# Performance work log

Hardware: AMD Instinct MI355X
Metric: run time of the kernel (lower is better)

Reference implementation:

```python
import math
import jax, jax.numpy as jnp
import numpy as np

B, T, C = 4, 2048, 1024
N_HEAD = 16
HEAD_DIM = C // N_HEAD

def setup_inputs() -> dict:
    key = jax.random.key(0)
    k0, k1, k2, k3, k4 = jax.random.split(key, 5)
    s = 1.0 / math.sqrt(C)
    return {
        "x": jax.random.normal(k0, (B, T, C), dtype=jnp.float32),
        "W_q": jax.random.normal(k1, (C, C), dtype=jnp.float32) * s,
        "W_k": jax.random.normal(k2, (C, C), dtype=jnp.float32) * s,
        "W_v": jax.random.normal(k3, (C, C), dtype=jnp.float32) * s,
        "W_o": jax.random.normal(k4, (C, C), dtype=jnp.float32) * s,
    }

def reference(x, W_q, W_k, W_v, W_o):
    b, t, c = x.shape
    h, hd = N_HEAD, HEAD_DIM
    # nn.Linear(y) = y @ W.T ; project and split heads -> [B, H, T, hd]
    q = (x @ W_q.T).reshape(b, t, h, hd).transpose(0, 2, 1, 3)
    k = (x @ W_k.T).reshape(b, t, h, hd).transpose(0, 2, 1, 3)
    v = (x @ W_v.T).reshape(b, t, h, hd).transpose(0, 2, 1, 3)
    # scores [B, H, T, T], causal mask, stable softmax
    attn = jnp.einsum('bhqd,bhkd->bhqk', q, k) / math.sqrt(hd)
    causal = jnp.tril(jnp.ones((t, t), dtype=bool))
    attn = jnp.where(causal[None, None], attn, -jnp.inf)
    attn = jax.nn.softmax(attn, axis=-1)
    out = jnp.einsum('bhqk,bhkd->bhqd', attn, v)
    out = out.transpose(0, 2, 1, 3).reshape(b, t, c)
    return out @ W_o.T
```

## Files before the change

kernel.cpp:

```cpp
#include <hip/hip_runtime.h>
#include <math.h>

#define Bsz 4
#define Tsz 2048
#define Csz 1024
#define NH  16
#define HD  64

typedef short bf16x8 __attribute__((ext_vector_type(8)));
typedef float f32x4  __attribute__((ext_vector_type(4)));
typedef unsigned short u16;
typedef unsigned int uint;

__device__ __forceinline__ u16 f2bf(float f) {
    union { float f; unsigned u; } v; v.f = f;
    unsigned r = v.u + 0x7fffu + ((v.u >> 16) & 1u);
    return (u16)(r >> 16);
}

__device__ __forceinline__ uint pkbf(float a, float b) {
    union { float f; uint u; } x, y; x.f = a; y.f = b;
    return ((x.u + 0x8000u) >> 16) | ((y.u + 0x8000u) & 0xFFFF0000u);
}

__device__ __forceinline__ void glds16(const u16* g, u16* l) {
    __builtin_amdgcn_global_load_lds(
        (const __attribute__((address_space(1))) void*)g,
        (__attribute__((address_space(3))) void*)l, 16, 0, 0);
}

__global__ void cast_kernel(const float* __restrict__ src, u16* __restrict__ dst, int n) {
    int i = (blockIdx.x * blockDim.x + threadIdx.x) * 8;
    if (i + 8 <= n) {
        float4 a = *(const float4*)(src + i);
        float4 b = *(const float4*)(src + i + 4);
        bf16x8 o;
        o[0] = (short)f2bf(a.x); o[1] = (short)f2bf(a.y);
        o[2] = (short)f2bf(a.z); o[3] = (short)f2bf(a.w);
        o[4] = (short)f2bf(b.x); o[5] = (short)f2bf(b.y);
        o[6] = (short)f2bf(b.z); o[7] = (short)f2bf(b.w);
        *(bf16x8*)(dst + i) = o;
    } else {
        for (; i < n; i++) dst[i] = f2bf(src[i]);
    }
}

__global__ void cast4_kernel(const float* __restrict__ s0, const float* __restrict__ s1,
                             const float* __restrict__ s2, const float* __restrict__ s3,
                             u16* __restrict__ dst) {
    const int NW = Csz * Csz;
    int i = (blockIdx.x * blockDim.x + threadIdx.x) * 8;
    int m = i >> 20;
    int local = i & (NW - 1);
    const float* src = (m == 0) ? s0 : (m == 1) ? s1 : (m == 2) ? s2 : s3;
    float4 a = *(const float4*)(src + local);
    float4 b = *(const float4*)(src + local + 4);
    bf16x8 o;
    o[0] = (short)f2bf(a.x); o[1] = (short)f2bf(a.y);
    o[2] = (short)f2bf(a.z); o[3] = (short)f2bf(a.w);
    o[4] = (short)f2bf(b.x); o[5] = (short)f2bf(b.y);
    o[6] = (short)f2bf(b.z); o[7] = (short)f2bf(b.w);
    *(bf16x8*)(dst + i) = o;
}


#define G2_SS 24576

#define G2_STAGEA(SLOT, KH, KT, PTR) {                                               \
    const int row_ = tid >> 2;                                                       \
    const int sc_ = (tid & 3) ^ ((row_ >> 1) & 3);                                   \
    glds16((PTR) + (size_t)row_ * 1024 + (KT) * 64 + (KH) * 32 + sc_ * 8,            \
           lds + (SLOT) * G2_SS + (KH) * 4096 + wave * 512); }

#define G2_STAGEB(SLOT, KH, KT, PTR) {                                               \
    _Pragma("unroll")                                                                \
    for (int rho = 0; rho < 2; rho++) {                                              \
        const int row_ = rho * 128 + (tid >> 2);                                     \
        const int sc_ = (tid & 3) ^ ((row_ >> 1) & 3);                               \
        glds16((PTR) + (size_t)row_ * 1024 + (KT) * 64 + (KH) * 32 + sc_ * 8,        \
               lds + (SLOT) * G2_SS + 8192 + (KH) * 8192 + rho * 4096 + wave * 512); } }

#define G2_PHASE(SLOT, KH, STAGE)                                                    \
    {                                                                                \
        __builtin_amdgcn_s_barrier();                                                \
        asm volatile("" ::: "memory");                                               \
        STAGE                                                                        \
        const u16* abase = lds + (SLOT) * G2_SS + (KH) * 4096;                       \
        const u16* bbase = lds + (SLOT) * G2_SS + 8192 + (KH) * 8192;                \
        bf16x8 afr[4], bfr[4];                                                       \
        _Pragma("unroll")                                                            \
        for (int i = 0; i < 4; i++) {                                                \
            const int ar = wrb + i * 16 + lr;                                        \
            afr[i] = *(const bf16x8*)(abase + ar * 32 +                              \
                                      ((lq ^ ((ar >> 1) & 3)) * 8));                 \
        }                                                                            \
        _Pragma("unroll")                                                            \
        for (int j = 0; j < 4; j++) {                                                \
            const int nr = wcb + j * 16 + lr;                                        \
            bfr[j] = *(const bf16x8*)(bbase + nr * 32 +                              \
                                      ((lq ^ ((nr >> 1) & 3)) * 8));                 \
        }                                                                            \
        asm volatile("" ::: "memory");                                               \
        __builtin_amdgcn_s_setprio(1);                                               \
        _Pragma("unroll")                                                            \
        for (int i = 0; i < 4; i++)                                                  \
            _Pragma("unroll")                                                        \
            for (int j = 0; j < 4; j++)                                              \
                acc[i][j] = __builtin_amdgcn_mfma_f32_16x16x32_bf16(                 \
                    afr[i], bfr[j], acc[i][j], 0, 0, 0);                             \
        __builtin_amdgcn_s_setprio(0);                                               \
    }

#define G2_VM(N) asm volatile("s_waitcnt vmcnt(" #N ")" ::: "memory")

#define G2_BODY(AP_, BP_)                                                            \
    __shared__ u16 lds[49152];                                                       \
    const int tid = threadIdx.x;                                                     \
    const int wave = tid >> 6, lane = tid & 63;                                      \
    const int lr = lane & 15, lq = lane >> 4;                                        \
    const int wrb = (wave >> 2) * 64, wcb = (wave & 3) * 64;                         \
    f32x4 acc[4][4] = {};                                                            \
    G2_STAGEA(0, 0, 0, AP_) G2_STAGEB(0, 0, 0, BP_)                                  \
    G2_STAGEA(0, 1, 0, AP_) G2_STAGEB(0, 1, 0, BP_)                                  \
    G2_STAGEA(1, 0, 1, AP_) G2_STAGEB(1, 0, 1, BP_)                                  \
    for (int t = 0; t < 16; t++) {                                                   \
        const int s = t & 1;                                                         \
        if (t == 15) { G2_VM(3); } else { G2_VM(6); }                                \
        G2_PHASE(s, 0, if (t < 15) { G2_STAGEA(s ^ 1, 1, t + 1, AP_)                 \
                                     G2_STAGEB(s ^ 1, 1, t + 1, BP_) })              \
        if (t == 15) { G2_VM(0); } else { G2_VM(6); }                                \
        G2_PHASE(s, 1, if (t < 14) { G2_STAGEA(s, 0, t + 2, AP_)                     \
                                     G2_STAGEB(s, 0, t + 2, BP_) })                  \
    }

__global__ __launch_bounds__(512, 2)
void gemm_qkv(const u16* __restrict__ A, const u16* __restrict__ Bm,
              u16* __restrict__ Qo, u16* __restrict__ Ko, u16* __restrict__ Vo,
              float qscale) {
    const int wg = blockIdx.x;
    const int chunk = wg & 7, pos = wg >> 3;
    const int m0 = ((chunk >> 1) * 16 + pos / 6) * 128;
    const int n0 = ((chunk & 1) * 6 + pos % 6) * 256;
    const u16* Ap = A  + (size_t)m0 * 1024;
    const u16* Bp = Bm + (size_t)n0 * 1024;

    G2_BODY(Ap, Bp)

    const int sel = n0 >> 10;
    if (sel == 2) {
        #pragma unroll
        for (int mi = 0; mi < 4; mi++) {
            #pragma unroll
            for (int ni = 0; ni < 4; ni++) {
                int m = m0 + wrb + mi * 16 + lq * 4;
                int b = m >> 11, tt = m & (Tsz - 1);
                int n = (n0 & 1023) + wcb + ni * 16 + lr;
                int h = n >> 6, d = n & (HD - 1);
                uint2 pk;
                pk.x = pkbf(acc[mi][ni][0], acc[mi][ni][1]);
                pk.y = pkbf(acc[mi][ni][2], acc[mi][ni][3]);
                *(uint2*)(&Vo[(((size_t)b * NH + h) * HD + d) * Tsz + tt]) = pk;
            }
        }
    } else {
        const float scale = (sel == 0) ? qscale : 1.0f;
        u16* dst = (sel == 0) ? Qo : Ko;
        #pragma unroll
        for (int mi = 0; mi < 4; mi++)
            #pragma unroll
            for (int ni = 0; ni < 4; ni++)
                #pragma unroll
                for (int r = 0; r < 4; r++) {
                    int m = m0 + wrb + mi * 16 + lq * 4 + r;
                    int n = (n0 & 1023) + wcb + ni * 16 + lr;
                    int b = m >> 11, tt = m & (Tsz - 1);
                    int h = n >> 6,  d = n & (HD - 1);
                    dst[(((size_t)b * NH + h) * Tsz + tt) * HD + d] = f2bf(acc[mi][ni][r] * scale);
                }
    }
}

__global__ __launch_bounds__(512, 2)
void gemm_out(const u16* __restrict__ A, const u16* __restrict__ Bm,
              float* __restrict__ out) {
    const int wg = blockIdx.x;
    const int chunk = wg & 7, pos = wg >> 3;
    const int m0 = (chunk * 8 + (pos >> 2)) * 128;
    const int n0 = (pos & 3) * 256;
    const u16* Ap = A  + (size_t)m0 * 1024;
    const u16* Bp = Bm + (size_t)n0 * 1024;

    G2_BODY(Ap, Bp)

    #pragma unroll
    for (int mi = 0; mi < 4; mi++)
        #pragma unroll
        for (int ni = 0; ni < 4; ni++)
            #pragma unroll
            for (int r = 0; r < 4; r++) {
                int m = m0 + wrb + mi * 16 + lq * 4 + r;
                int n = n0 + wcb + ni * 16 + lr;
                out[(size_t)m * Csz + n] = acc[mi][ni][r];
            }
}

#define LDT  72
#define LDTP 68

__global__ __launch_bounds__(256, 4)
void attn_kernel(const u16* __restrict__ Q, const u16* __restrict__ Kb,
                 const u16* __restrict__ Vt, u16* __restrict__ O) {
    __shared__ u16 sK[64 * LDT];
    __shared__ u16 sV[64 * LDT];
    __shared__ u16 sP[4][16 * LDTP];
    const int tid  = threadIdx.x;
    const int wave = tid >> 6, lane = tid & 63;
    const int lr = lane & 15, lq = lane >> 4;
    const int bh = blockIdx.x;
    const int qa = blockIdx.y;
    const int qc = 31 - qa;
    const int ta = qa * 64, tc = qc * 64;

    const u16* Qp = Q  + (size_t)bh * Tsz * HD;
    const u16* Kp = Kb + (size_t)bh * Tsz * HD;
    const u16* Vp = Vt + (size_t)bh * HD * Tsz;

    bf16x8 qfA0 = *(const bf16x8*)(Qp + (size_t)(ta + wave * 16 + lr) * HD + lq * 8);
    bf16x8 qfA1 = *(const bf16x8*)(Qp + (size_t)(ta + wave * 16 + lr) * HD + 32 + lq * 8);
    bf16x8 qfC0 = *(const bf16x8*)(Qp + (size_t)(tc + wave * 16 + lr) * HD + lq * 8);
    bf16x8 qfC1 = *(const bf16x8*)(Qp + (size_t)(tc + wave * 16 + lr) * HD + 32 + lq * 8);

    f32x4 accOA[4] = {}, accOC[4] = {};
    f32x4 accLA = {}, accLC = {};

    bf16x8 ones;
    #pragma unroll
    for (int i = 0; i < 8; i++) ones[i] = (short)0x3F80;

    const int strow = tid >> 3;
    const int stcol = (tid & 7) * 8;
    const u16* gK0 = Kp + (size_t)strow * HD + stcol;
    const u16* gK1 = gK0 + 32 * HD;
    const u16* gV0 = Vp + (size_t)strow * Tsz + stcol;
    const u16* gV1 = gV0 + 32 * Tsz;
    u16* lK0 = sK + strow * LDT + stcol;  u16* lK1 = lK0 + 32 * LDT;
    u16* lV0 = sV + strow * LDT + stcol;  u16* lV1 = lV0 + 32 * LDT;

    bf16x8 pK0 = *(const bf16x8*)(gK0);
    bf16x8 pK1 = *(const bf16x8*)(gK1);
    bf16x8 pV0 = *(const bf16x8*)(gV0);
    bf16x8 pV1 = *(const bf16x8*)(gV1);

#define PROCESS(T0, QF0, QF1, ACCO, ACCL, DIAG)                                       \
    {                                                                                 \
        f32x4 accS[4];                                                                \
        __builtin_amdgcn_s_setprio(1);                                                \
        _Pragma("unroll")                                                             \
        for (int j = 0; j < 4; j++) {                                                 \
            bf16x8 b0 = *(const bf16x8*)(sK + (j * 16 + lr) * LDT + lq * 8);          \
            bf16x8 b1 = *(const bf16x8*)(sK + (j * 16 + lr) * LDT + 32 + lq * 8);     \
            f32x4 z = {};                                                             \
            z = __builtin_amdgcn_mfma_f32_16x16x32_bf16(QF0, b0, z, 0, 0, 0);         \
            z = __builtin_amdgcn_mfma_f32_16x16x32_bf16(QF1, b1, z, 0, 0, 0);         \
            accS[j] = z;                                                              \
        }                                                                             \
        __builtin_amdgcn_s_setprio(0);                                                \
        _Pragma("unroll")                                                             \
        for (int r = 0; r < 4; r++) {                                                 \
            const int rowg = (T0) + wave * 16 + lq * 4 + r;                           \
            _Pragma("unroll")                                                         \
            for (int j = 0; j < 4; j++) {                                             \
                float v = accS[j][r];                                                 \
                if (DIAG && (kb * 64 + j * 16 + lr > rowg)) v = -200.0f;              \
                union { float f; uint u; } e;                                         \
                e.f = __builtin_amdgcn_exp2f(v);                                      \
                sP[wave][(lq * 4 + r) * LDTP + j * 16 + lr] = (u16)(e.u >> 16);       \
            }                                                                         \
        }                                                                             \
        __builtin_amdgcn_s_setprio(1);                                                \
        _Pragma("unroll")                                                             \
        for (int ks = 0; ks < 2; ks++) {                                              \
            bf16x8 pf = *(const bf16x8*)(&sP[wave][0] + lr * LDTP + ks * 32 + lq * 8);\
            ACCL = __builtin_amdgcn_mfma_f32_16x16x32_bf16(pf, ones, ACCL, 0, 0, 0);  \
            _Pragma("unroll")                                                         \
            for (int j = 0; j < 4; j++) {                                             \
                bf16x8 vf = *(const bf16x8*)(sV + (j * 16 + lr) * LDT + ks * 32 + lq * 8); \
                ACCO[j] = __builtin_amdgcn_mfma_f32_16x16x32_bf16(pf, vf, ACCO[j], 0, 0, 0); \
            }                                                                         \
        }                                                                             \
        __builtin_amdgcn_s_setprio(0);                                                \
    }

    for (int kb = 0; kb <= qc; kb++) {
        __syncthreads();
        *(bf16x8*)lK0 = pK0; *(bf16x8*)lK1 = pK1;
        *(bf16x8*)lV0 = pV0; *(bf16x8*)lV1 = pV1;
        __syncthreads();
        if (kb < qc) {
            pK0 = *(const bf16x8*)(gK0 + (size_t)(kb + 1) * 64 * HD);
            pK1 = *(const bf16x8*)(gK1 + (size_t)(kb + 1) * 64 * HD);
            pV0 = *(const bf16x8*)(gV0 + (kb + 1) * 64);
            pV1 = *(const bf16x8*)(gV1 + (kb + 1) * 64);
        }
        if (kb < qa) {
            PROCESS(ta, qfA0, qfA1, accOA, accLA, 0)
            PROCESS(tc, qfC0, qfC1, accOC, accLC, 0)
        } else if (kb == qa) {
            PROCESS(ta, qfA0, qfA1, accOA, accLA, 1)
            PROCESS(tc, qfC0, qfC1, accOC, accLC, 0)
        } else if (kb < qc) {
            PROCESS(tc, qfC0, qfC1, accOC, accLC, 0)
        } else {
            PROCESS(tc, qfC0, qfC1, accOC, accLC, 1)
        }
    }
#undef PROCESS

    const int b = bh >> 4, h = bh & 15;
    #pragma unroll
    for (int j = 0; j < 4; j++) {
        #pragma unroll
        for (int r = 0; r < 4; r++) {
            int t = wave * 16 + lq * 4 + r;
            int d = j * 16 + lr;
            O[((size_t)b * Tsz + ta + t) * Csz + h * HD + d] = f2bf(accOA[j][r] / accLA[r]);
            O[((size_t)b * Tsz + tc + t) * Csz + h * HD + d] = f2bf(accOC[j][r] / accLC[r]);
        }
    }
}

extern "C" void kernel_launch(void* const* d_in, const int* in_sizes, int n_in,
                              void* d_out, int out_size, void* d_ws, size_t ws_size,
                              hipStream_t stream) {
    const float* x  = (const float*)d_in[0];
    const float* Wq = (const float*)d_in[1];
    const float* Wk = (const float*)d_in[2];
    const float* Wv = (const float*)d_in[3];
    const float* Wo = (const float*)d_in[4];
    float* out = (float*)d_out;

    const size_t NX = (size_t)Bsz * Tsz * Csz;
    const size_t NW = (size_t)Csz * Csz;

    char* ws = (char*)d_ws;
    u16* xb   = (u16*)ws; ws += NX * 2;
    u16* wqkv = (u16*)ws; ws += 3 * NW * 2;
    u16* wob  = (u16*)ws; ws += NW * 2;
    u16* qbuf = (u16*)ws; ws += NX * 2;
    u16* kbuf = (u16*)ws; ws += NX * 2;
    u16* vtb  = (u16*)ws; ws += NX * 2;
    u16* abuf = (u16*)ws; ws += NX * 2;

    cast_kernel<<<dim3((unsigned)(NX / 2048)), 256, 0, stream>>>(x, xb, (int)NX);
    cast4_kernel<<<dim3((unsigned)(4 * NW / 2048)), 256, 0, stream>>>(Wq, Wk, Wv, Wo, wqkv);

    const float qscale = 0.125f * 1.44269504088896340736f;
    gemm_qkv<<<dim3(768), 512, 0, stream>>>(xb, wqkv, qbuf, kbuf, vtb, qscale);

    attn_kernel<<<dim3(Bsz * NH, 16), 256, 0, stream>>>(qbuf, kbuf, vtb, abuf);

    gemm_out<<<dim3(256), 512, 0, stream>>>(abuf, wob, out);
}
```

Before: 258.1 us.

## Merge cast kernels, drop setprio hints, collapse attention branch dispatch

Fuses the activation and weight bf16 cast kernels into a single launch that picks its source by global index, removing one kernel launch. It also removes the s_setprio priority hints around the MFMA phases in the attention inner loop. The four-way branch over diagonal/non-diagonal tiles is replaced by two PROCESS calls with a runtime diagonal flag, which shrinks code size but makes the mask check a runtime condition instead of a compile-time constant.

```diff
diff --git a/kernel.cpp b/kernel.cpp
--- a/kernel.cpp
+++ b/kernel.cpp
@@ -29,38 +29,32 @@
         (__attribute__((address_space(3))) void*)l, 16, 0, 0);
 }
 
-__global__ void cast_kernel(const float* __restrict__ src, u16* __restrict__ dst, int n) {
-    int i = (blockIdx.x * blockDim.x + threadIdx.x) * 8;
-    if (i + 8 <= n) {
-        float4 a = *(const float4*)(src + i);
-        float4 b = *(const float4*)(src + i + 4);
-        bf16x8 o;
-        o[0] = (short)f2bf(a.x); o[1] = (short)f2bf(a.y);
-        o[2] = (short)f2bf(a.z); o[3] = (short)f2bf(a.w);
-        o[4] = (short)f2bf(b.x); o[5] = (short)f2bf(b.y);
-        o[6] = (short)f2bf(b.z); o[7] = (short)f2bf(b.w);
-        *(bf16x8*)(dst + i) = o;
+__global__ void cast_all(const float* __restrict__ x,
+                         const float* __restrict__ s0, const float* __restrict__ s1,
+                         const float* __restrict__ s2, const float* __restrict__ s3,
+                         u16* __restrict__ xb, u16* __restrict__ wdst) {
+    const int NW = Csz * Csz;
+    const size_t NX = (size_t)Bsz * Tsz * Csz;
+    size_t i = ((size_t)blockIdx.x * blockDim.x + threadIdx.x) * 8;
+    const float* src;
+    u16* dst;
+    if (i < NX) {
+        src = x + i; dst = xb + i;
     } else {
-        for (; i < n; i++) dst[i] = f2bf(src[i]);
-    }
-}
-
-__global__ void cast4_kernel(const float* __restrict__ s0, const float* __restrict__ s1,
-                             const float* __restrict__ s2, const float* __restrict__ s3,
-                             u16* __restrict__ dst) {
-    const int NW = Csz * Csz;
-    int i = (blockIdx.x * blockDim.x + threadIdx.x) * 8;
-    int m = i >> 20;
-    int local = i & (NW - 1);
-    const float* src = (m == 0) ? s0 : (m == 1) ? s1 : (m == 2) ? s2 : s3;
-    float4 a = *(const float4*)(src + local);
-    float4 b = *(const float4*)(src + local + 4);
+        size_t j = i - NX;
+        int m = (int)(j >> 20);
+        size_t local = j & (NW - 1);
+        src = ((m == 0) ? s0 : (m == 1) ? s1 : (m == 2) ? s2 : s3) + local;
+        dst = wdst + j;
+    }
+    float4 a = *(const float4*)(src);
+    float4 b = *(const float4*)(src + 4);
     bf16x8 o;
     o[0] = (short)f2bf(a.x); o[1] = (short)f2bf(a.y);
     o[2] = (short)f2bf(a.z); o[3] = (short)f2bf(a.w);
     o[4] = (short)f2bf(b.x); o[5] = (short)f2bf(b.y);
     o[6] = (short)f2bf(b.z); o[7] = (short)f2bf(b.w);
-    *(bf16x8*)(dst + i) = o;
+    *(bf16x8*)(dst) = o;
 }
 
 
@@ -254,7 +248,6 @@
 #define PROCESS(T0, QF0, QF1, ACCO, ACCL, DIAG)                                       \
     {                                                                                 \
         f32x4 accS[4];                                                                \
-        __builtin_amdgcn_s_setprio(1);                                                \
         _Pragma("unroll")                                                             \
         for (int j = 0; j < 4; j++) {                                                 \
             bf16x8 b0 = *(const bf16x8*)(sK + (j * 16 + lr) * LDT + lq * 8);          \
@@ -264,7 +257,6 @@
             z = __builtin_amdgcn_mfma_f32_16x16x32_bf16(QF1, b1, z, 0, 0, 0);         \
             accS[j] = z;                                                              \
         }                                                                             \
-        __builtin_amdgcn_s_setprio(0);                                                \
         _Pragma("unroll")                                                             \
         for (int r = 0; r < 4; r++) {                                                 \
             const int rowg = (T0) + wave * 16 + lq * 4 + r;                           \
@@ -277,7 +269,6 @@
                 sP[wave][(lq * 4 + r) * LDTP + j * 16 + lr] = (u16)(e.u >> 16);       \
             }                                                                         \
         }                                                                             \
-        __builtin_amdgcn_s_setprio(1);                                                \
         _Pragma("unroll")                                                             \
         for (int ks = 0; ks < 2; ks++) {                                              \
             bf16x8 pf = *(const bf16x8*)(&sP[wave][0] + lr * LDTP + ks * 32 + lq * 8);\
@@ -288,7 +279,6 @@
                 ACCO[j] = __builtin_amdgcn_mfma_f32_16x16x32_bf16(pf, vf, ACCO[j], 0, 0, 0); \
             }                                                                         \
         }                                                                             \
-        __builtin_amdgcn_s_setprio(0);                                                \
     }
 
     for (int kb = 0; kb <= qc; kb++) {
@@ -302,17 +292,8 @@
             pV0 = *(const bf16x8*)(gV0 + (kb + 1) * 64);
             pV1 = *(const bf16x8*)(gV1 + (kb + 1) * 64);
         }
-        if (kb < qa) {
-            PROCESS(ta, qfA0, qfA1, accOA, accLA, 0)
-            PROCESS(tc, qfC0, qfC1, accOC, accLC, 0)
-        } else if (kb == qa) {
-            PROCESS(ta, qfA0, qfA1, accOA, accLA, 1)
-            PROCESS(tc, qfC0, qfC1, accOC, accLC, 0)
-        } else if (kb < qc) {
-            PROCESS(tc, qfC0, qfC1, accOC, accLC, 0)
-        } else {
-            PROCESS(tc, qfC0, qfC1, accOC, accLC, 1)
-        }
+        if (kb <= qa) PROCESS(ta, qfA0, qfA1, accOA, accLA, (kb == qa));
+        PROCESS(tc, qfC0, qfC1, accOC, accLC, (kb == qc));
     }
 #undef PROCESS
 
@@ -351,8 +332,8 @@
     u16* vtb  = (u16*)ws; ws += NX * 2;
     u16* abuf = (u16*)ws; ws += NX * 2;
 
-    cast_kernel<<<dim3((unsigned)(NX / 2048)), 256, 0, stream>>>(x, xb, (int)NX);
-    cast4_kernel<<<dim3((unsigned)(4 * NW / 2048)), 256, 0, stream>>>(Wq, Wk, Wv, Wo, wqkv);
+    cast_all<<<dim3((unsigned)((NX + 4 * NW) / 2048)), 256, 0, stream>>>(
+        x, Wq, Wk, Wv, Wo, xb, wqkv);
 
     const float qscale = 0.125f * 1.44269504088896340736f;
     gemm_qkv<<<dim3(768), 512, 0, stream>>>(xb, wqkv, qbuf, kbuf, vtb, qscale);
```

Result: faster. 241.9 us, median of 2 (-6.3%).
